# Kernel optimization log

Hardware: AMD Instinct MI355X
Metric: run time of the kernel (lower is better)

## Reference

```python
import jax, jax.numpy as jnp
import numpy as np

N, F, FH, H = 4096, 512, 64, 8  # nodes, in-features, per-head out-features, heads
ALPHA = 0.2  # LeakyReLU slope


def setup_inputs() -> dict:
    key = jax.random.key(0)
    ks = jax.random.split(key, 6)
    X = jax.random.normal(ks[0], (N, F), dtype=jnp.float32)
    A = (jax.random.uniform(ks[1], (N, N)) < 0.02).astype(jnp.float32)
    glorot_w = (2.0 / (F + FH)) ** 0.5
    glorot_a = (2.0 / (FH + 1)) ** 0.5
    W = jax.random.normal(ks[2], (H, F, FH), dtype=jnp.float32) * glorot_w
    a_self = jax.random.normal(ks[3], (H, FH), dtype=jnp.float32) * glorot_a
    a_neigh = jax.random.normal(ks[4], (H, FH), dtype=jnp.float32) * glorot_a
    b = jnp.zeros((H, FH), dtype=jnp.float32)
    return {"X": X, "A": A, "W": W, "a_self": a_self, "a_neigh": a_neigh, "b": b}


def reference(X, A, W, a_self, a_neigh, b):
    # per-head linear projection: [H, N, FH]
    feats = jnp.einsum('nf,hfo->hno', X, W)
    s_self = jnp.einsum('hno,ho->hn', feats, a_self)    # [H, N]
    s_neigh = jnp.einsum('hno,ho->hn', feats, a_neigh)  # [H, N]
    # additive logits: self_i + neigh_j -> [H, N, N]
    dense = s_self[:, :, None] + s_neigh[:, None, :]
    dense = jnp.where(dense > 0, dense, ALPHA * dense)  # LeakyReLU(0.2)
    dense = dense * A[None, :, :]                       # multiplicative adjacency (as in source)
    attn = jax.nn.softmax(dense, axis=-1)               # full-row softmax (as in source)
    # dropout is identity at inference
    out = jnp.einsum('hij,hjo->hio', attn, feats) + b[:, None, :]  # [H, N, FH]
    out = jnp.transpose(out, (1, 0, 2)).reshape(N, H * FH)         # concat heads
    return jax.nn.relu(out)
```

## Files before the change

kernel.cpp:

```cpp
#include <hip/hip_runtime.h>
#include <hip/hip_bf16.h>

#define N_NODES 4096
#define F_IN 512
#define FHD 64
#define H_HEADS 8
#define C_OUT 512
#define ALPHA 0.2f
#define MAXE 192

typedef __attribute__((ext_vector_type(8))) short bf16x8;
typedef __attribute__((ext_vector_type(4))) float f32x4;

static __device__ __forceinline__ unsigned short f2bf(float f) {
  __hip_bfloat16 h = __float2bfloat16(f);
  union { __hip_bfloat16 h; unsigned short u; } cvt;
  cvt.h = h;
  return cvt.u;
}
static __device__ __forceinline__ float bf2f(unsigned short u) {
  return __uint_as_float(((unsigned)u) << 16);
}

__global__ __launch_bounds__(256) void prep_kernel(
    const float* __restrict__ A, const float* __restrict__ X,
    const float* __restrict__ W, unsigned short* __restrict__ edges,
    int* __restrict__ degs, unsigned short* __restrict__ Xb,
    unsigned short* __restrict__ WbT, float* __restrict__ colsum) {
  __shared__ int wave_tot[4];
  __shared__ float sT[64][65];
  const int bid = blockIdx.x;
  const int tid = threadIdx.x;

  if (bid < N_NODES) {
    const int i = bid;
    const int wid = tid >> 6, lane = tid & 63;
    const float4* __restrict__ Arow4 =
        reinterpret_cast<const float4*>(A + (size_t)i * N_NODES);
    float4 v[4];
#pragma unroll
    for (int q = 0; q < 4; ++q) v[q] = Arow4[tid * 4 + q];
    int mask16 = 0;
#pragma unroll
    for (int q = 0; q < 4; ++q) {
      mask16 |= (v[q].x != 0.f) ? (1 << (q * 4 + 0)) : 0;
      mask16 |= (v[q].y != 0.f) ? (1 << (q * 4 + 1)) : 0;
      mask16 |= (v[q].z != 0.f) ? (1 << (q * 4 + 2)) : 0;
      mask16 |= (v[q].w != 0.f) ? (1 << (q * 4 + 3)) : 0;
    }
    int cnt = __popc(mask16);
    int inc = cnt;
#pragma unroll
    for (int s = 1; s < 64; s <<= 1) {
      int t = __shfl_up(inc, s, 64);
      if (lane >= s) inc += t;
    }
    if (lane == 63) wave_tot[wid] = inc;
    __syncthreads();
    int wprefix = 0, tot = 0;
#pragma unroll
    for (int w = 0; w < 4; ++w) {
      int t = wave_tot[w];
      if (w < wid) wprefix += t;
      tot += t;
    }
    int pos = wprefix + inc - cnt;
    const int jbase = tid * 16;
    unsigned short* __restrict__ erow = edges + (size_t)i * MAXE;
    while (mask16) {
      int k = __ffs(mask16) - 1;
      mask16 &= mask16 - 1;
      if (pos < MAXE) erow[pos] = (unsigned short)(jbase + k);
      ++pos;
    }
    if (tid == 0) degs[i] = tot < MAXE ? tot : MAXE;
  } else if (bid < N_NODES + 2048) {
    int idx = (bid - N_NODES) * 256 + tid;
    float4 v = reinterpret_cast<const float4*>(X)[idx];
    ushort4 u;
    u.x = f2bf(v.x); u.y = f2bf(v.y); u.z = f2bf(v.z); u.w = f2bf(v.w);
    reinterpret_cast<ushort4*>(Xb)[idx] = u;
  } else if (bid < N_NODES + 2048 + 64) {
    const int b2 = bid - (N_NODES + 2048);
    const int fblk = b2 & 7, h = b2 >> 3;
#pragma unroll
    for (int i = 0; i < 16; ++i) {
      int idx = tid + i * 256;
      int f = idx >> 6, o = idx & 63;
      sT[f][o] = W[((size_t)h * F_IN + fblk * 64 + f) * FHD + o];
    }
    __syncthreads();
#pragma unroll
    for (int i = 0; i < 16; ++i) {
      int idx = tid + i * 256;
      int o = idx >> 6, f = idx & 63;
      WbT[(size_t)h * FHD * F_IN + (size_t)o * F_IN + fblk * 64 + f] =
          f2bf(sT[f][o]);
    }
  } else {
    colsum[tid] = 0.f;
    colsum[tid + 256] = 0.f;
  }
}

__global__ __launch_bounds__(256) void gemm_feats_mfma_kernel(
    const unsigned short* __restrict__ Xb, const unsigned short* __restrict__ WbT,
    const float* __restrict__ a_self, const float* __restrict__ a_neigh,
    unsigned short* __restrict__ featsb,
    float* __restrict__ s_self, float* __restrict__ s_neigh,
    float* __restrict__ colsum) {
  const int h = blockIdx.y;
  const int n0 = blockIdx.x * 128;
  __shared__ unsigned short sX[2][128 * 40];
  __shared__ unsigned short sW[2][64 * 40];
  __shared__ float sred[4][64];
  const int tid = threadIdx.x;
  const int wid = tid >> 6, lane = tid & 63;
  const int l15 = lane & 15, l4 = lane >> 4;

  const int xrow = tid >> 1, xoff = (tid & 1) * 16;
  const unsigned short* xsrc = Xb + (size_t)(n0 + xrow) * F_IN + xoff;
  const int sxoff = xrow * 40 + xoff;
  const int wn = tid >> 2, woff = (tid & 3) * 8;
  const unsigned short* wsrc = WbT + ((size_t)h * FHD + wn) * F_IN + woff;
  const int swoff = wn * 40 + woff;

  f32x4 acc[2][4];
#pragma unroll
  for (int i = 0; i < 2; ++i)
#pragma unroll
    for (int j = 0; j < 4; ++j) acc[i][j] = (f32x4){0.f, 0.f, 0.f, 0.f};

  {
    bf16x8 x0 = *(const bf16x8*)(xsrc);
    bf16x8 x1 = *(const bf16x8*)(xsrc + 8);
    bf16x8 w0 = *(const bf16x8*)(wsrc);
    *(bf16x8*)&sX[0][sxoff] = x0;
    *(bf16x8*)&sX[0][sxoff + 8] = x1;
    *(bf16x8*)&sW[0][swoff] = w0;
  }
  __syncthreads();

  const int arow0 = (wid * 32 + l15) * 40 + l4 * 8;
  const int arow1 = (wid * 32 + 16 + l15) * 40 + l4 * 8;
  int cur = 0;
  for (int s = 0; s < 16; ++s) {
    bf16x8 px0, px1, pw0;
    const bool pf = (s < 15);
    if (pf) {
      const int k = (s + 1) * 32;
      px0 = *(const bf16x8*)(xsrc + k);
      px1 = *(const bf16x8*)(xsrc + k + 8);
      pw0 = *(const bf16x8*)(wsrc + k);
    }
    bf16x8 a0 = *(const bf16x8*)&sX[cur][arow0];
    bf16x8 a1 = *(const bf16x8*)&sX[cur][arow1];
#pragma unroll
    for (int tn = 0; tn < 4; ++tn) {
      bf16x8 b = *(const bf16x8*)&sW[cur][(tn * 16 + l15) * 40 + l4 * 8];
      acc[0][tn] =
          __builtin_amdgcn_mfma_f32_16x16x32_bf16(a0, b, acc[0][tn], 0, 0, 0);
      acc[1][tn] =
          __builtin_amdgcn_mfma_f32_16x16x32_bf16(a1, b, acc[1][tn], 0, 0, 0);
    }
    if (pf) {
      *(bf16x8*)&sX[cur ^ 1][sxoff] = px0;
      *(bf16x8*)&sX[cur ^ 1][sxoff + 8] = px1;
      *(bf16x8*)&sW[cur ^ 1][swoff] = pw0;
      __syncthreads();
      cur ^= 1;
    }
  }

  float aS[4], aN[4];
#pragma unroll
  for (int tn = 0; tn < 4; ++tn) {
    aS[tn] = a_self[h * FHD + tn * 16 + l15];
    aN[tn] = a_neigh[h * FHD + tn * 16 + l15];
  }
#pragma unroll
  for (int tm = 0; tm < 2; ++tm) {
#pragma unroll
    for (int r = 0; r < 4; ++r) {
      const int grow = n0 + wid * 32 + tm * 16 + l4 * 4 + r;
#pragma unroll
      for (int tn = 0; tn < 4; ++tn)
        featsb[(size_t)grow * C_OUT + h * FHD + tn * 16 + l15] =
            f2bf(acc[tm][tn][r]);
      float ps = 0.f, pn = 0.f;
#pragma unroll
      for (int tn = 0; tn < 4; ++tn) {
        float v = acc[tm][tn][r];
        ps = fmaf(v, aS[tn], ps);
        pn = fmaf(v, aN[tn], pn);
      }
#pragma unroll
      for (int sh = 1; sh < 16; sh <<= 1) {
        ps += __shfl_xor(ps, sh, 64);
        pn += __shfl_xor(pn, sh, 64);
      }
      if (l15 == 0) {
        s_self[grow * 8 + h] = ps;
        s_neigh[grow * 8 + h] = pn;
      }
    }
  }

  float psum[4];
#pragma unroll
  for (int tn = 0; tn < 4; ++tn) {
    float s = 0.f;
#pragma unroll
    for (int tm = 0; tm < 2; ++tm)
#pragma unroll
      for (int r = 0; r < 4; ++r) s += acc[tm][tn][r];
    s += __shfl_xor(s, 16, 64);
    s += __shfl_xor(s, 32, 64);
    psum[tn] = s;
  }
  if (l4 == 0) {
#pragma unroll
    for (int tn = 0; tn < 4; ++tn) sred[wid][tn * 16 + l15] = psum[tn];
  }
  __syncthreads();
  if (tid < 64) {
    float s = sred[0][tid] + sred[1][tid] + sred[2][tid] + sred[3][tid];
    atomicAdd(&colsum[h * FHD + tid], s);
  }
}

__global__ __launch_bounds__(256) void attn_kernel(
    const unsigned short* __restrict__ edges, const int* __restrict__ degs,
    const unsigned short* __restrict__ featsb,
    const float* __restrict__ s_self, const float* __restrict__ s_neigh,
    const float* __restrict__ colsum, const float* __restrict__ bias,
    float* __restrict__ out) {
  const int i = blockIdx.x;
  const int tid = threadIdx.x;
  const int wid = tid >> 6, lane = tid & 63;
  __shared__ int s_idx[MAXE];
  __shared__ float s_w[MAXE][9];
  __shared__ float sh_self[8];
  __shared__ float sh_e0[8], sh_invZ[8];

  const int deg = degs[i];
  if (tid < 8) sh_self[tid] = s_self[i * 8 + tid];
  if (tid < deg) s_idx[tid] = edges[(size_t)i * MAXE + tid];
  __syncthreads();

  for (int k = tid; k < deg * 8; k += 256) {
    int e = k >> 3, h = k & 7;
    int j = s_idx[e];
    float l = sh_self[h] + s_neigh[j * 8 + h];
    s_w[e][h] = l > 0.f ? l : ALPHA * l;
  }
  __syncthreads();

#pragma unroll
  for (int p = 0; p < 2; ++p) {
    const int h = wid * 2 + p;
    float m = -1e30f;
    for (int e = lane; e < deg; e += 64) m = fmaxf(m, s_w[e][h]);
#pragma unroll
    for (int s = 32; s > 0; s >>= 1) m = fmaxf(m, __shfl_xor(m, s, 64));
    m = fmaxf(m, 0.0f);
    float e0 = __expf(-m);
    float zs = 0.f;
    for (int e = lane; e < deg; e += 64) {
      float w = __expf(s_w[e][h] - m);
      s_w[e][h] = w - e0;
      zs += w;
    }
#pragma unroll
    for (int s = 32; s > 0; s >>= 1) zs += __shfl_xor(zs, s, 64);
    if (lane == 0) {
      sh_e0[h] = e0;
      sh_invZ[h] = 1.0f / (zs + (float)(N_NODES - deg) * e0);
    }
  }
  __syncthreads();

  const int h = tid >> 5;
  const float e0 = sh_e0[h], invZ = sh_invZ[h];
  const float2 cs = *reinterpret_cast<const float2*>(&colsum[tid * 2]);
  const ushort2* __restrict__ fb = reinterpret_cast<const ushort2*>(featsb);
  float ax0 = e0 * cs.x, ay0 = e0 * cs.y;
  float ax1 = 0.f, ay1 = 0.f, ax2 = 0.f, ay2 = 0.f, ax3 = 0.f, ay3 = 0.f;
  int e = 0;
  for (; e + 3 < deg; e += 4) {
    int j0 = s_idx[e], j1 = s_idx[e + 1], j2 = s_idx[e + 2], j3 = s_idx[e + 3];
    float w0 = s_w[e][h], w1 = s_w[e + 1][h];
    float w2 = s_w[e + 2][h], w3 = s_w[e + 3][h];
    ushort2 u0 = fb[(size_t)j0 * 256 + tid];
    ushort2 u1 = fb[(size_t)j1 * 256 + tid];
    ushort2 u2 = fb[(size_t)j2 * 256 + tid];
    ushort2 u3 = fb[(size_t)j3 * 256 + tid];
    ax0 = fmaf(w0, bf2f(u0.x), ax0);
    ay0 = fmaf(w0, bf2f(u0.y), ay0);
    ax1 = fmaf(w1, bf2f(u1.x), ax1);
    ay1 = fmaf(w1, bf2f(u1.y), ay1);
    ax2 = fmaf(w2, bf2f(u2.x), ax2);
    ay2 = fmaf(w2, bf2f(u2.y), ay2);
    ax3 = fmaf(w3, bf2f(u3.x), ax3);
    ay3 = fmaf(w3, bf2f(u3.y), ay3);
  }
  for (; e < deg; ++e) {
    float w0 = s_w[e][h];
    ushort2 u0 = fb[(size_t)s_idx[e] * 256 + tid];
    ax0 = fmaf(w0, bf2f(u0.x), ax0);
    ay0 = fmaf(w0, bf2f(u0.y), ay0);
  }
  const float2 bb = *reinterpret_cast<const float2*>(&bias[tid * 2]);
  float vx = ((ax0 + ax1) + (ax2 + ax3)) * invZ + bb.x;
  float vy = ((ay0 + ay1) + (ay2 + ay3)) * invZ + bb.y;
  float2 o;
  o.x = vx > 0.f ? vx : 0.f;
  o.y = vy > 0.f ? vy : 0.f;
  *reinterpret_cast<float2*>(&out[(size_t)i * C_OUT + tid * 2]) = o;
}

extern "C" void kernel_launch(void* const* d_in, const int* in_sizes, int n_in,
                              void* d_out, int out_size, void* d_ws, size_t ws_size,
                              hipStream_t stream) {
  const float* X = (const float*)d_in[0];
  const float* A = (const float*)d_in[1];
  const float* W = (const float*)d_in[2];
  const float* a_self = (const float*)d_in[3];
  const float* a_neigh = (const float*)d_in[4];
  const float* b = (const float*)d_in[5];
  float* out = (float*)d_out;

  char* ws = (char*)d_ws;
  unsigned short* featsb = (unsigned short*)ws;
  char* p = ws + (size_t)N_NODES * C_OUT * 2;
  float* s_self = (float*)p;  p += N_NODES * H_HEADS * 4;
  float* s_neigh = (float*)p; p += N_NODES * H_HEADS * 4;
  float* colsum = (float*)p;  p += C_OUT * 4;
  int* degs = (int*)p;        p += N_NODES * 4;
  unsigned short* edges = (unsigned short*)p;
  p += (size_t)N_NODES * MAXE * 2;
  unsigned short* WbT = (unsigned short*)p;

  unsigned short* Xb = (unsigned short*)d_out;

  prep_kernel<<<N_NODES + 2048 + 64 + 1, 256, 0, stream>>>(
      A, X, W, edges, degs, Xb, WbT, colsum);
  gemm_feats_mfma_kernel<<<dim3(32, 8), 256, 0, stream>>>(
      Xb, WbT, a_self, a_neigh, featsb, s_self, s_neigh, colsum);
  attn_kernel<<<N_NODES, 256, 0, stream>>>(edges, degs, featsb, s_self,
                                           s_neigh, colsum, b, out);
}
```

Baseline: 59.14 us.

## Fuse adjacency compaction into attention kernel and retile feature GEMM

Moves the per-row adjacency scan and edge-list compaction out of the prep kernel and into the attention kernel, so neighbor indices go straight to shared memory instead of through a global edges/degs buffer. The feature GEMM is retiled from 128-row to 64-row blocks with a 64-wide K step, doubling the grid to 512 blocks for better occupancy. The trade-off is that the A row read now sits on the attention kernel's critical path, where it may not overlap with the gather work.

```diff
diff --git a/kernel.cpp b/kernel.cpp
--- a/kernel.cpp
+++ b/kernel.cpp
@@ -22,66 +22,21 @@
   return __uint_as_float(((unsigned)u) << 16);
 }
 
-__global__ __launch_bounds__(256) void prep_kernel(
-    const float* __restrict__ A, const float* __restrict__ X,
-    const float* __restrict__ W, unsigned short* __restrict__ edges,
-    int* __restrict__ degs, unsigned short* __restrict__ Xb,
-    unsigned short* __restrict__ WbT, float* __restrict__ colsum) {
-  __shared__ int wave_tot[4];
+__global__ __launch_bounds__(256) void conv_kernel(
+    const float* __restrict__ X, const float* __restrict__ W,
+    unsigned short* __restrict__ Xb, unsigned short* __restrict__ WbT,
+    float* __restrict__ colsum) {
   __shared__ float sT[64][65];
   const int bid = blockIdx.x;
   const int tid = threadIdx.x;
-
-  if (bid < N_NODES) {
-    const int i = bid;
-    const int wid = tid >> 6, lane = tid & 63;
-    const float4* __restrict__ Arow4 =
-        reinterpret_cast<const float4*>(A + (size_t)i * N_NODES);
-    float4 v[4];
-#pragma unroll
-    for (int q = 0; q < 4; ++q) v[q] = Arow4[tid * 4 + q];
-    int mask16 = 0;
-#pragma unroll
-    for (int q = 0; q < 4; ++q) {
-      mask16 |= (v[q].x != 0.f) ? (1 << (q * 4 + 0)) : 0;
-      mask16 |= (v[q].y != 0.f) ? (1 << (q * 4 + 1)) : 0;
-      mask16 |= (v[q].z != 0.f) ? (1 << (q * 4 + 2)) : 0;
-      mask16 |= (v[q].w != 0.f) ? (1 << (q * 4 + 3)) : 0;
-    }
-    int cnt = __popc(mask16);
-    int inc = cnt;
-#pragma unroll
-    for (int s = 1; s < 64; s <<= 1) {
-      int t = __shfl_up(inc, s, 64);
-      if (lane >= s) inc += t;
-    }
-    if (lane == 63) wave_tot[wid] = inc;
-    __syncthreads();
-    int wprefix = 0, tot = 0;
-#pragma unroll
-    for (int w = 0; w < 4; ++w) {
-      int t = wave_tot[w];
-      if (w < wid) wprefix += t;
-      tot += t;
-    }
-    int pos = wprefix + inc - cnt;
-    const int jbase = tid * 16;
-    unsigned short* __restrict__ erow = edges + (size_t)i * MAXE;
-    while (mask16) {
-      int k = __ffs(mask16) - 1;
-      mask16 &= mask16 - 1;
-      if (pos < MAXE) erow[pos] = (unsigned short)(jbase + k);
-      ++pos;
-    }
-    if (tid == 0) degs[i] = tot < MAXE ? tot : MAXE;
-  } else if (bid < N_NODES + 2048) {
-    int idx = (bid - N_NODES) * 256 + tid;
+  if (bid < 2048) {
+    int idx = bid * 256 + tid;
     float4 v = reinterpret_cast<const float4*>(X)[idx];
     ushort4 u;
     u.x = f2bf(v.x); u.y = f2bf(v.y); u.z = f2bf(v.z); u.w = f2bf(v.w);
     reinterpret_cast<ushort4*>(Xb)[idx] = u;
-  } else if (bid < N_NODES + 2048 + 64) {
-    const int b2 = bid - (N_NODES + 2048);
+  } else if (bid < 2048 + 64) {
+    const int b2 = bid - 2048;
     const int fblk = b2 & 7, h = b2 >> 3;
 #pragma unroll
     for (int i = 0; i < 16; ++i) {
@@ -110,63 +65,55 @@
     float* __restrict__ s_self, float* __restrict__ s_neigh,
     float* __restrict__ colsum) {
   const int h = blockIdx.y;
-  const int n0 = blockIdx.x * 128;
-  __shared__ unsigned short sX[2][128 * 40];
-  __shared__ unsigned short sW[2][64 * 40];
+  const int n0 = blockIdx.x * 64;
+  __shared__ unsigned short sX[2][64 * 72];
+  __shared__ unsigned short sW[2][64 * 72];
   __shared__ float sred[4][64];
   const int tid = threadIdx.x;
   const int wid = tid >> 6, lane = tid & 63;
   const int l15 = lane & 15, l4 = lane >> 4;
 
-  const int xrow = tid >> 1, xoff = (tid & 1) * 16;
-  const unsigned short* xsrc = Xb + (size_t)(n0 + xrow) * F_IN + xoff;
-  const int sxoff = xrow * 40 + xoff;
-  const int wn = tid >> 2, woff = (tid & 3) * 8;
-  const unsigned short* wsrc = WbT + ((size_t)h * FHD + wn) * F_IN + woff;
-  const int swoff = wn * 40 + woff;
-
-  f32x4 acc[2][4];
-#pragma unroll
-  for (int i = 0; i < 2; ++i)
-#pragma unroll
-    for (int j = 0; j < 4; ++j) acc[i][j] = (f32x4){0.f, 0.f, 0.f, 0.f};
-
-  {
-    bf16x8 x0 = *(const bf16x8*)(xsrc);
-    bf16x8 x1 = *(const bf16x8*)(xsrc + 8);
-    bf16x8 w0 = *(const bf16x8*)(wsrc);
-    *(bf16x8*)&sX[0][sxoff] = x0;
-    *(bf16x8*)&sX[0][sxoff + 8] = x1;
-    *(bf16x8*)&sW[0][swoff] = w0;
-  }
-  __syncthreads();
-
-  const int arow0 = (wid * 32 + l15) * 40 + l4 * 8;
-  const int arow1 = (wid * 32 + 16 + l15) * 40 + l4 * 8;
+  const int row = tid >> 2, seg = (tid & 3) * 16;
+  const unsigned short* xsrc = Xb + (size_t)(n0 + row) * F_IN + seg;
+  const unsigned short* wsrc = WbT + ((size_t)h * FHD + row) * F_IN + seg;
+  const int soff = row * 72 + seg;
+
+  f32x4 acc[4];
+#pragma unroll
+  for (int j = 0; j < 4; ++j) acc[j] = (f32x4){0.f, 0.f, 0.f, 0.f};
+
+  *(bf16x8*)&sX[0][soff] = *(const bf16x8*)(xsrc);
+  *(bf16x8*)&sX[0][soff + 8] = *(const bf16x8*)(xsrc + 8);
+  *(bf16x8*)&sW[0][soff] = *(const bf16x8*)(wsrc);
+  *(bf16x8*)&sW[0][soff + 8] = *(const bf16x8*)(wsrc + 8);
+  __syncthreads();
+
   int cur = 0;
-  for (int s = 0; s < 16; ++s) {
-    bf16x8 px0, px1, pw0;
-    const bool pf = (s < 15);
+  for (int s = 0; s < 8; ++s) {
+    bf16x8 px0, px1, pw0, pw1;
+    const bool pf = (s < 7);
     if (pf) {
-      const int k = (s + 1) * 32;
+      const int k = (s + 1) * 64;
       px0 = *(const bf16x8*)(xsrc + k);
       px1 = *(const bf16x8*)(xsrc + k + 8);
       pw0 = *(const bf16x8*)(wsrc + k);
-    }
-    bf16x8 a0 = *(const bf16x8*)&sX[cur][arow0];
-    bf16x8 a1 = *(const bf16x8*)&sX[cur][arow1];
-#pragma unroll
-    for (int tn = 0; tn < 4; ++tn) {
-      bf16x8 b = *(const bf16x8*)&sW[cur][(tn * 16 + l15) * 40 + l4 * 8];
-      acc[0][tn] =
-          __builtin_amdgcn_mfma_f32_16x16x32_bf16(a0, b, acc[0][tn], 0, 0, 0);
-      acc[1][tn] =
-          __builtin_amdgcn_mfma_f32_16x16x32_bf16(a1, b, acc[1][tn], 0, 0, 0);
+      pw1 = *(const bf16x8*)(wsrc + k + 8);
+    }
+#pragma unroll
+    for (int kk = 0; kk < 2; ++kk) {
+      bf16x8 a = *(const bf16x8*)&sX[cur][(wid * 16 + l15) * 72 + kk * 32 + l4 * 8];
+#pragma unroll
+      for (int tn = 0; tn < 4; ++tn) {
+        bf16x8 b = *(const bf16x8*)&sW[cur][(tn * 16 + l15) * 72 + kk * 32 + l4 * 8];
+        acc[tn] =
+            __builtin_amdgcn_mfma_f32_16x16x32_bf16(a, b, acc[tn], 0, 0, 0);
+      }
     }
     if (pf) {
-      *(bf16x8*)&sX[cur ^ 1][sxoff] = px0;
-      *(bf16x8*)&sX[cur ^ 1][sxoff + 8] = px1;
-      *(bf16x8*)&sW[cur ^ 1][swoff] = pw0;
+      *(bf16x8*)&sX[cur ^ 1][soff] = px0;
+      *(bf16x8*)&sX[cur ^ 1][soff + 8] = px1;
+      *(bf16x8*)&sW[cur ^ 1][soff] = pw0;
+      *(bf16x8*)&sW[cur ^ 1][soff + 8] = pw1;
       __syncthreads();
       cur ^= 1;
     }
@@ -179,41 +126,34 @@
     aN[tn] = a_neigh[h * FHD + tn * 16 + l15];
   }
 #pragma unroll
-  for (int tm = 0; tm < 2; ++tm) {
-#pragma unroll
-    for (int r = 0; r < 4; ++r) {
-      const int grow = n0 + wid * 32 + tm * 16 + l4 * 4 + r;
-#pragma unroll
-      for (int tn = 0; tn < 4; ++tn)
-        featsb[(size_t)grow * C_OUT + h * FHD + tn * 16 + l15] =
-            f2bf(acc[tm][tn][r]);
-      float ps = 0.f, pn = 0.f;
-#pragma unroll
-      for (int tn = 0; tn < 4; ++tn) {
-        float v = acc[tm][tn][r];
-        ps = fmaf(v, aS[tn], ps);
-        pn = fmaf(v, aN[tn], pn);
-      }
-#pragma unroll
-      for (int sh = 1; sh < 16; sh <<= 1) {
-        ps += __shfl_xor(ps, sh, 64);
-        pn += __shfl_xor(pn, sh, 64);
-      }
-      if (l15 == 0) {
-        s_self[grow * 8 + h] = ps;
-        s_neigh[grow * 8 + h] = pn;
-      }
+  for (int r = 0; r < 4; ++r) {
+    const int grow = n0 + wid * 16 + l4 * 4 + r;
+#pragma unroll
+    for (int tn = 0; tn < 4; ++tn)
+      featsb[(size_t)grow * C_OUT + h * FHD + tn * 16 + l15] =
+          f2bf(acc[tn][r]);
+    float ps = 0.f, pn = 0.f;
+#pragma unroll
+    for (int tn = 0; tn < 4; ++tn) {
+      float v = acc[tn][r];
+      ps = fmaf(v, aS[tn], ps);
+      pn = fmaf(v, aN[tn], pn);
+    }
+#pragma unroll
+    for (int sh = 1; sh < 16; sh <<= 1) {
+      ps += __shfl_xor(ps, sh, 64);
+      pn += __shfl_xor(pn, sh, 64);
+    }
+    if (l15 == 0) {
+      s_self[grow * 8 + h] = ps;
+      s_neigh[grow * 8 + h] = pn;
     }
   }
 
   float psum[4];
 #pragma unroll
   for (int tn = 0; tn < 4; ++tn) {
-    float s = 0.f;
-#pragma unroll
-    for (int tm = 0; tm < 2; ++tm)
-#pragma unroll
-      for (int r = 0; r < 4; ++r) s += acc[tm][tn][r];
+    float s = acc[tn][0] + acc[tn][1] + acc[tn][2] + acc[tn][3];
     s += __shfl_xor(s, 16, 64);
     s += __shfl_xor(s, 32, 64);
     psum[tn] = s;
@@ -230,8 +170,7 @@
 }
 
 __global__ __launch_bounds__(256) void attn_kernel(
-    const unsigned short* __restrict__ edges, const int* __restrict__ degs,
-    const unsigned short* __restrict__ featsb,
+    const float* __restrict__ A, const unsigned short* __restrict__ featsb,
     const float* __restrict__ s_self, const float* __restrict__ s_neigh,
     const float* __restrict__ colsum, const float* __restrict__ bias,
     float* __restrict__ out) {
@@ -240,12 +179,50 @@
   const int wid = tid >> 6, lane = tid & 63;
   __shared__ int s_idx[MAXE];
   __shared__ float s_w[MAXE][9];
+  __shared__ int wave_tot[4];
   __shared__ float sh_self[8];
   __shared__ float sh_e0[8], sh_invZ[8];
 
-  const int deg = degs[i];
   if (tid < 8) sh_self[tid] = s_self[i * 8 + tid];
-  if (tid < deg) s_idx[tid] = edges[(size_t)i * MAXE + tid];
+
+  const float4* __restrict__ Arow4 =
+      reinterpret_cast<const float4*>(A + (size_t)i * N_NODES);
+  float4 v[4];
+#pragma unroll
+  for (int q = 0; q < 4; ++q) v[q] = Arow4[tid * 4 + q];
+  int mask16 = 0;
+#pragma unroll
+  for (int q = 0; q < 4; ++q) {
+    mask16 |= (v[q].x != 0.f) ? (1 << (q * 4 + 0)) : 0;
+    mask16 |= (v[q].y != 0.f) ? (1 << (q * 4 + 1)) : 0;
+    mask16 |= (v[q].z != 0.f) ? (1 << (q * 4 + 2)) : 0;
+    mask16 |= (v[q].w != 0.f) ? (1 << (q * 4 + 3)) : 0;
+  }
+  int cnt = __popc(mask16);
+  int inc = cnt;
+#pragma unroll
+  for (int s = 1; s < 64; s <<= 1) {
+    int t = __shfl_up(inc, s, 64);
+    if (lane >= s) inc += t;
+  }
+  if (lane == 63) wave_tot[wid] = inc;
+  __syncthreads();
+  int wprefix = 0, tot = 0;
+#pragma unroll
+  for (int w = 0; w < 4; ++w) {
+    int t = wave_tot[w];
+    if (w < wid) wprefix += t;
+    tot += t;
+  }
+  int pos = wprefix + inc - cnt;
+  const int jbase = tid * 16;
+  while (mask16) {
+    int k = __ffs(mask16) - 1;
+    mask16 &= mask16 - 1;
+    if (pos < MAXE) s_idx[pos] = jbase + k;
+    ++pos;
+  }
+  const int deg = tot < MAXE ? tot : MAXE;
   __syncthreads();
 
   for (int k = tid; k < deg * 8; k += 256) {
@@ -336,17 +313,13 @@
   float* s_self = (float*)p;  p += N_NODES * H_HEADS * 4;
   float* s_neigh = (float*)p; p += N_NODES * H_HEADS * 4;
   float* colsum = (float*)p;  p += C_OUT * 4;
-  int* degs = (int*)p;        p += N_NODES * 4;
-  unsigned short* edges = (unsigned short*)p;
-  p += (size_t)N_NODES * MAXE * 2;
   unsigned short* WbT = (unsigned short*)p;
 
   unsigned short* Xb = (unsigned short*)d_out;
 
-  prep_kernel<<<N_NODES + 2048 + 64 + 1, 256, 0, stream>>>(
-      A, X, W, edges, degs, Xb, WbT, colsum);
-  gemm_feats_mfma_kernel<<<dim3(32, 8), 256, 0, stream>>>(
+  conv_kernel<<<2048 + 64 + 1, 256, 0, stream>>>(X, W, Xb, WbT, colsum);
+  gemm_feats_mfma_kernel<<<dim3(64, 8), 256, 0, stream>>>(
       Xb, WbT, a_self, a_neigh, featsb, s_self, s_neigh, colsum);
-  attn_kernel<<<N_NODES, 256, 0, stream>>>(edges, degs, featsb, s_self,
-                                           s_neigh, colsum, b, out);
-}
+  attn_kernel<<<N_NODES, 256, 0, stream>>>(A, featsb, s_self, s_neigh, colsum,
+                                           b, out);
+}
```

Result: slower. 60.51 us (+2.3%).
